# Kernel tuning notes

Hardware: AMD Instinct MI355X
Metric: run time of the kernel (lower is better)

Reference implementation:

```python
import jax, jax.numpy as jnp
import numpy as np

B, N, M, D, H, DK = 4, 2048, 1024, 512, 8, 64  # H*DK == D (required by residual E + E_)
SCALE = 1.0 / np.sqrt(DK)
NEG = -9e15


def setup_inputs() -> dict:
    key = jax.random.key(0)
    ks = jax.random.split(key, 24)
    def W(k, din, dout):
        return (0.02 * jax.random.truncated_normal(k, -2.0, 2.0, (din, dout))).astype(jnp.float32)
    inp = {
        'X': jax.random.normal(ks[0], (B, N, D), jnp.float32),
        'incidence_matrix': jax.random.randint(ks[1], (B, N, M), 0, 2, jnp.int32),
        'attn_bias': jnp.zeros((1,), jnp.float32),
        'E': jax.random.normal(ks[2], (B, M, D), jnp.float32),
        'Wqn': W(ks[3], D, H * DK), 'bqn': jnp.zeros((H * DK,), jnp.float32),
        'Wkn': W(ks[4], D, H * DK), 'bkn': jnp.zeros((H * DK,), jnp.float32),
        'Wvn': W(ks[5], D, H * DK), 'bvn': jnp.zeros((H * DK,), jnp.float32),
        'Wqe': W(ks[6], D, H * DK), 'bqe': jnp.zeros((H * DK,), jnp.float32),
        'Wke': W(ks[7], D, H * DK), 'bke': jnp.zeros((H * DK,), jnp.float32),
        'Wve': W(ks[8], D, H * DK), 'bve': jnp.zeros((H * DK,), jnp.float32),
        'Wm1': W(ks[9], D, D), 'bm1': jnp.zeros((D,), jnp.float32),
        'Wm2': W(ks[10], D, D), 'bm2': jnp.zeros((D,), jnp.float32),
        'g_ln': jnp.ones((D,), jnp.float32), 'b_ln': jnp.zeros((D,), jnp.float32),
    }
    return inp


def _heads(x, Wt, b):
    # [B, L, D] -> [B, H, L, DK]
    b_, l_ = x.shape[0], x.shape[1]
    return (x @ Wt + b).reshape(b_, l_, H, DK).transpose(0, 2, 1, 3)


def _merge(x):
    # [B, H, L, DK] -> [B, L, H*DK]
    b_, _, l_, _ = x.shape
    return x.transpose(0, 2, 1, 3).reshape(b_, l_, H * DK)


def _layernorm(x, g, b, eps=1e-7):
    mu = jnp.mean(x, axis=-1, keepdims=True)
    var = jnp.var(x, axis=-1, keepdims=True)
    return (x - mu) * jax.lax.rsqrt(var + eps) * g + b


def _gelu(x):
    return jax.nn.gelu(x, approximate=False)


def reference(X, incidence_matrix, attn_bias, E,
              Wqn, bqn, Wkn, bkn, Wvn, bvn,
              Wqe, bqe, Wke, bke, Wve, bve,
              Wm1, bm1, Wm2, bm2, g_ln, b_ln):
    q_n = _heads(X, Wqn, bqn)   # [B,H,N,DK]
    k_n = _heads(X, Wkn, bkn)
    v_n = _heads(X, Wvn, bvn)
    q_e = _heads(E, Wqe, bqe)   # [B,H,M,DK]

    # edge attends over nodes: [B,H,M,N], masked by incidence^T
    att_e = jnp.einsum('bhmd,bhnd->bhmn', q_e, k_n) * SCALE
    mask_e = (incidence_matrix > 0).transpose(0, 2, 1)[:, None, :, :]  # [B,1,M,N]
    att_e = jnp.where(mask_e, att_e, NEG)
    w_e = jax.nn.softmax(att_e, axis=-1)
    E_ = _gelu(jnp.einsum('bhmn,bhnd->bhmd', w_e, v_n))
    E_ = _merge(E_)                                   # [B,M,D]
    E_ = _layernorm(E + E_, g_ln, b_ln)
    E_ = _gelu(E_ @ Wm1 + bm1) @ Wm2 + bm2            # MLP

    k_e = _heads(E_, Wke, bke)  # [B,H,M,DK]
    v_e = _heads(E_, Wve, bve)

    # node attends over edges: [B,H,N,M], masked by incidence
    att_n = jnp.einsum('bhnd,bhmd->bhnm', q_n, k_e) * SCALE
    mask_n = (incidence_matrix > 0)[:, None, :, :]    # [B,1,N,M]
    att_n = jnp.where(mask_n, att_n, NEG)
    w_n = jax.nn.softmax(att_n, axis=-1)
    X_ = _gelu(jnp.einsum('bhnm,bhmd->bhnd', w_n, v_e))
    X_ = _merge(X_)                                   # [B,N,D]
    return (X_, E_)
```

## Files before the change

kernel.cpp:

```cpp
#include <hip/hip_runtime.h>

typedef unsigned short u16;
typedef unsigned int   u32;
typedef unsigned long long u64;

typedef __attribute__((ext_vector_type(8))) short  bf16x8;
typedef __attribute__((ext_vector_type(16))) float f32x16;

#define SC2 0.1803368801111243f
#define CS2 11.541560327111707f

__device__ __forceinline__ float bf2f(u16 h) { return __uint_as_float(((u32)h) << 16); }
__device__ __forceinline__ u16 f2bf(float f) {
  u32 u = __float_as_uint(f);
  return (u16)((u + 0x7FFFu + ((u >> 16) & 1u)) >> 16);
}
__device__ __forceinline__ float gelu_f(float x) {
  return 0.5f * x * (1.0f + erff(x * 0.70710678118654752440f));
}
__device__ __forceinline__ void dma16(const u16* g, u16* l) {
  __builtin_amdgcn_global_load_lds(
      (const __attribute__((address_space(1))) u32*)g,
      (__attribute__((address_space(3))) u32*)l, 16, 0, 0);
}
__device__ __forceinline__ u32 cvtpk(float lo, float hi) {
  u32 r;
  asm("v_cvt_pk_bf16_f32 %0, %1, %2" : "=v"(r) : "v"(lo), "v"(hi));
  return r;
}

__global__ void detect_dtype(const u16* __restrict__ X, u32* __restrict__ flag) {
  int lane = threadIdx.x;
  int bad = 0;
  #pragma unroll
  for (int i = 0; i < 8; ++i) {
    u16 v = X[i * 64 + lane];
    int e = (v >> 7) & 0xFF;
    if (e >= 0x88) bad++;
  }
  #pragma unroll
  for (int o = 1; o < 64; o <<= 1) bad += __shfl_xor(bad, o);
  if (lane == 0) *flag = (bad > 16) ? 1u : 0u;
}

__global__ __launch_bounds__(256) void fill_diag(u32* __restrict__ out, float base,
                                                 const u32* __restrict__ flag) {
  float v = base + (*flag ? 4000.0f : 0.0f);
  u16 h = f2bf(v);
  out[blockIdx.x * 256 + threadIdx.x] = (u32)h | ((u32)h << 16);
}

__global__ __launch_bounds__(256) void prep_all(
    const void* __restrict__ Xsrc, const void* __restrict__ Esrc,
    const int* __restrict__ inc,
    const void* w0, const void* w1, const void* w2, const void* w3,
    const void* w4, const void* w5, const void* w6, const void* w7,
    const void* p0, const void* p1, const void* p2, const void* p3, const void* p4,
    const void* p5, const void* p6, const void* p7, const void* p8, const void* p9,
    u16* __restrict__ XB, u16* __restrict__ EB, u16* __restrict__ WT,
    u16* __restrict__ VEC, u16* __restrict__ T0, u16* __restrict__ T1,
    const u32* __restrict__ flag) {
  int bi = blockIdx.x;
  int t = threadIdx.x;
  int fl = (int)(*flag);

  if (bi < 3072) {
    const void* src = bi < 2048 ? Xsrc : Esrc;
    u16* dst = bi < 2048 ? XB : EB;
    int base = bi < 2048 ? bi : bi - 2048;
    int i = (base * 256 + t) * 8;
    if (fl) {
      const float* s = (const float*)src + i;
      float4 a = *(const float4*)s;
      float4 b = *(const float4*)(s + 4);
      uint4 o;
      o.x = (u32)f2bf(a.x) | ((u32)f2bf(a.y) << 16);
      o.y = (u32)f2bf(a.z) | ((u32)f2bf(a.w) << 16);
      o.z = (u32)f2bf(b.x) | ((u32)f2bf(b.y) << 16);
      o.w = (u32)f2bf(b.z) | ((u32)f2bf(b.w) << 16);
      *(uint4*)(dst + i) = o;
    } else {
      *(uint4*)(dst + i) = *(const uint4*)((const u16*)src + i);
    }
  } else if (bi < 5120) {
    const void* wsrc[8] = {w0, w1, w2, w3, w4, w5, w6, w7};
    __shared__ u16 tile[32][33];
    int r = bi - 3072;
    int bx = (r & 15) * 32, by = ((r >> 4) & 15) * 32, z = r >> 8;
    const void* W = wsrc[z];
    u16* Wt = WT + (size_t)z * 262144;
    int tx = t & 31, ty = t >> 5;
    #pragma unroll
    for (int i = 0; i < 4; ++i) {
      int rr = ty + 8 * i;
      size_t src = (size_t)(by + rr) * 512 + bx + tx;
      tile[rr][tx] = fl ? f2bf(((const float*)W)[src]) : ((const u16*)W)[src];
    }
    __syncthreads();
    #pragma unroll
    for (int i = 0; i < 4; ++i) {
      int rr = ty + 8 * i;
      Wt[(size_t)(bx + rr) * 512 + by + tx] = tile[tx][rr];
    }
  } else if (bi == 5120) {
    const void* ps[10] = {p0, p1, p2, p3, p4, p5, p6, p7, p8, p9};
    for (int idx = t; idx < 5120; idx += 256) {
      int slot = idx >> 9, off = idx & 511;
      u16 v;
      if (fl) v = f2bf(((const float*)ps[slot])[off]);
      else    v = ((const u16*)ps[slot])[off];
      VEC[idx] = v;
    }
  } else {
    int r = bi - 5121;
    int qt32 = r & 31, nt = (r >> 5) & 31, b = r >> 10;
    int f = t >> 6, l = t & 63;
    int nl = l & 31, h = l >> 5;
    int key  = ((f >> 1) << 5) + nl;
    int qrow = ((f & 1) << 4) + h * 8;
    const int* src = inc + ((size_t)(b * 2048 + nt * 64 + key)) * 1024 + qt32 * 32 + qrow;
    uint4 a = *(const uint4*)src;
    uint4 c = *(const uint4*)(src + 4);
    uint4 o;
    o.x = (a.x ? 0u : 0xC480u) | (a.y ? 0u : 0xC4800000u);
    o.y = (a.z ? 0u : 0xC480u) | (a.w ? 0u : 0xC4800000u);
    o.z = (c.x ? 0u : 0xC480u) | (c.y ? 0u : 0xC4800000u);
    o.w = (c.z ? 0u : 0xC480u) | (c.w ? 0u : 0xC4800000u);
    u16* dst = (b < 2 ? T0 + (size_t)b * 2097152 : T1 + (size_t)(b - 2) * 2097152)
               + ((size_t)nt * 32 + qt32) * 2048 + t * 8;
    *(uint4*)dst = o;
  }
}

__global__ __launch_bounds__(256) void transposeV(const u16* __restrict__ Vp,
                                                  u16* __restrict__ VT, int Lk) {
  __shared__ u16 tile[64][72];
  int t = threadIdx.x;
  int nt = blockIdx.x;
  int bh = blockIdx.y;
  int nw = Lk >> 6;
  const u16* src = Vp + ((size_t)bh * Lk + nt * 64) * 64;
  int key = t >> 2, seg = t & 3;
  int dc0 = seg * 2, dc1 = seg * 2 + 1;
  uint4 a  = *(const uint4*)(src + key * 64 + ((dc0 ^ (key & 7)) << 3));
  uint4 b2 = *(const uint4*)(src + key * 64 + ((dc1 ^ (key & 7)) << 3));
  *(uint4*)&tile[key][dc0 * 8] = a;
  *(uint4*)&tile[key][dc1 * 8] = b2;
  __syncthreads();
  int d = t >> 2;
  u32 wb[8];
  #pragma unroll
  for (int i = 0; i < 8; ++i) {
    u32 lo = tile[seg * 16 + 2 * i][d];
    u32 hi = tile[seg * 16 + 2 * i + 1][d];
    wb[i] = lo | (hi << 16);
  }
  u16* base = VT + (((size_t)bh * nw + nt) * 64 + d) * 64;
  int kc0 = seg * 2, kc1 = seg * 2 + 1;
  uint4 o0; o0.x = wb[0]; o0.y = wb[1]; o0.z = wb[2]; o0.w = wb[3];
  uint4 o1; o1.x = wb[4]; o1.y = wb[5]; o1.z = wb[6]; o1.w = wb[7];
  *(uint4*)(base + ((kc0 ^ (d & 7)) << 3)) = o0;
  *(uint4*)(base + ((kc1 ^ (d & 7)) << 3)) = o1;
}

__global__ __launch_bounds__(256) void inc_tiles_node(const int* __restrict__ inc,
                                                      u16* __restrict__ T0,
                                                      u16* __restrict__ T1) {
  int qt32 = blockIdx.x, nt = blockIdx.y, b = blockIdx.z;
  int t = threadIdx.x;
  int f = t >> 6, l = t & 63;
  int nl = l & 31, h = l >> 5;
  int key  = ((f >> 1) << 5) + nl;
  int qrow = ((f & 1) << 4) + h * 8;
  const int* src = inc + ((size_t)(b * 2048 + qt32 * 32 + qrow)) * 1024 + nt * 64 + key;
  u16 o[8];
  #pragma unroll
  for (int e = 0; e < 8; ++e)
    o[e] = src[(size_t)e * 1024] ? (u16)0 : (u16)0xC480;
  uint4 ov;
  ov.x = (u32)o[0] | ((u32)o[1] << 16);
  ov.y = (u32)o[2] | ((u32)o[3] << 16);
  ov.z = (u32)o[4] | ((u32)o[5] << 16);
  ov.w = (u32)o[6] | ((u32)o[7] << 16);
  u16* dst = (b < 3 ? T0 + (size_t)b * 2097152 : T1)
             + ((size_t)nt * 64 + qt32) * 2048 + t * 8;
  *(uint4*)dst = ov;
}

__global__ __launch_bounds__(256) void gemm_tiled(const u16* __restrict__ A,
                                                  const u16* __restrict__ Wt0, u32 wtStride,
                                                  const u16* __restrict__ bias0, u32 bStride,
                                                  u16* __restrict__ C0, u32 cStride,
                                                  int act, int blocksPerMat,
                                                  u32 modeMask, int lkshift,
                                                  void* __restrict__ out2, size_t out2_off,
                                                  const u16* __restrict__ A3,
                                                  const u32* __restrict__ flag) {
  __shared__ u16 As[2][8192];
  __shared__ u16 Bs[2][8192];
  int wid = (blockIdx.x & 7) * (int)(gridDim.x >> 3) + (blockIdx.x >> 3);
  int mat = wid / blocksPerMat;
  int blk = wid % blocksPerMat;
  const u16* Wt = Wt0 + (size_t)mat * wtStride;
  const u16* bias = bias0 + (size_t)mat * bStride;
  u16* C = C0 + (size_t)mat * cStride;
  int mode = (modeMask >> mat) & 1u;
  int f32o = out2 ? (int)(*flag) : 0;
  const u16* Am = (A3 && mat == 3) ? A3 : A;
  int tm = blk >> 2, tn = blk & 3;
  int m0 = tm * 128, n0 = tn * 128;

  int t = threadIdx.x;
  int wave = t >> 6, lane = t & 63;
  int nl = lane & 31, h32 = lane >> 5;
  int wm = wave >> 1, wn = wave & 1;

  int srow = lane >> 3;
  int gch  = (lane & 7) ^ srow;
  const u16* Ab = Am + ((size_t)m0 + wave * 32) * 512 + (size_t)srow * 512 + gch * 8;
  const u16* Bb = Wt + ((size_t)n0 + wave * 32) * 512 + (size_t)srow * 512 + gch * 8;
  u16* AsW = &As[0][0] + wave * 32 * 64;
  u16* BsW = &Bs[0][0] + wave * 32 * 64;

  #pragma unroll
  for (int c = 0; c < 4; ++c) {
    dma16(Ab + (size_t)c * 8 * 512, AsW + c * 8 * 64);
    dma16(Bb + (size_t)c * 8 * 512, BsW + c * 8 * 64);
  }
  __syncthreads();

  f32x16 a00 = {}, a01 = {}, a10 = {}, a11 = {};

  for (int kk = 0; kk < 8; ++kk) {
    int buf = kk & 1;
    if (kk + 1 < 8) {
      int k0n = (kk + 1) * 64;
      u16* AD = &As[buf ^ 1][0] + wave * 32 * 64;
      u16* BD = &Bs[buf ^ 1][0] + wave * 32 * 64;
      #pragma unroll
      for (int c = 0; c < 4; ++c) {
        dma16(Ab + (size_t)c * 8 * 512 + k0n, AD + c * 8 * 64);
        dma16(Bb + (size_t)c * 8 * 512 + k0n, BD + c * 8 * 64);
      }
    }
    const u16* Ab_s = &As[buf][0];
    const u16* Bb_s = &Bs[buf][0];
    int ar0 = wm * 64 + nl, ar1 = wm * 64 + 32 + nl;
    int br0 = wn * 64 + nl, br1 = wn * 64 + 32 + nl;
    #pragma unroll
    for (int ks = 0; ks < 4; ++ks) {
      int sw = (((ks * 2 + h32) ^ (nl & 7)) << 3);
      bf16x8 fa0 = *(const bf16x8*)(Ab_s + ar0 * 64 + sw);
      bf16x8 fa1 = *(const bf16x8*)(Ab_s + ar1 * 64 + sw);
      bf16x8 fb0 = *(const bf16x8*)(Bb_s + br0 * 64 + sw);
      bf16x8 fb1 = *(const bf16x8*)(Bb_s + br1 * 64 + sw);
      a00 = __builtin_amdgcn_mfma_f32_32x32x16_bf16(fa0, fb0, a00, 0, 0, 0);
      a01 = __builtin_amdgcn_mfma_f32_32x32x16_bf16(fa0, fb1, a01, 0, 0, 0);
      a10 = __builtin_amdgcn_mfma_f32_32x32x16_bf16(fa1, fb0, a10, 0, 0, 0);
      a11 = __builtin_amdgcn_mfma_f32_32x32x16_bf16(fa1, fb1, a11, 0, 0, 0);
    }
    __syncthreads();
  }

  int nw = 1 << (lkshift - 6);
  #pragma unroll
  for (int am = 0; am < 2; ++am) {
    #pragma unroll
    for (int bn = 0; bn < 2; ++bn) {
      const f32x16* accp = am == 0 ? (bn == 0 ? &a00 : &a01)
                                   : (bn == 0 ? &a10 : &a11);
      f32x16 acc = *accp;
      int cn = n0 + wn * 64 + bn * 32 + nl;
      float bv = bf2f(bias[cn]);
      #pragma unroll
      for (int g = 0; g < 16; ++g) {
        int rm = m0 + wm * 64 + am * 32 + (g & 3) + 8 * (g >> 2) + 4 * h32;
        float v = acc[g] + bv;
        if (act) v = gelu_f(v);
        if (mode) {
          int bb = rm >> lkshift;
          int key = rm & ((1 << lkshift) - 1);
          int nt = key >> 6, kl = key & 63;
          int d = cn & 63;
          size_t ad = ((((size_t)bb * 8 + (cn >> 6)) * nw + nt) * 64 + kl) * 64
                      + (((d >> 3) ^ (kl & 7)) << 3) + (d & 7);
          C[ad] = f2bf(v);
        } else {
          size_t ad = (size_t)rm * 512 + cn;
          C[ad] = f2bf(v);
          if (out2) {
            if (f32o) ((float*)out2)[out2_off + ad] = v;
            else      ((u16*)out2)[out2_off + ad] = f2bf(v);
          }
        }
      }
    }
  }
}

__global__ __launch_bounds__(256, 4) void flash_mfma(
    const u16* __restrict__ Q,
    const u16* __restrict__ Kp,
    const u16* __restrict__ VTp,
    const u16* __restrict__ IncA,
    const u16* __restrict__ IncB,
    int nbA,
    void* __restrict__ Outv,
    u16* __restrict__ Opart, float* __restrict__ Lpart,
    int Lq, int Lk, int splits, int is_final, const u32* __restrict__ flag) {
  __shared__ u16 K_s[3][4096];
  __shared__ u16 V_s[3][4096];
  __shared__ u16 P_s[4][2048];

  int t = threadIdx.x;
  int wave = t >> 6, lane = t & 63;
  int nl = lane & 31, h32 = lane >> 5;
  int qtiles = Lq >> 7;
  int nwords = Lk >> 6;
  int chunk = (int)(gridDim.x >> 3);
  int wid = (blockIdx.x & 7) * chunk + (blockIdx.x >> 3);
  int r2 = wid % (qtiles * 32);
  int split = wid / (qtiles * 32);
  int qt = r2 % qtiles;
  int bh = r2 / qtiles;
  int h = bh & 7, b = bh >> 3;
  int row0 = qt * 128 + wave * 32;
  int per = nwords / splits;
  int tile0 = split * per;
  int f32o = is_final ? (int)(*flag) : 0;

  bf16x8 qf[4];
  {
    const u16* qp = Q + ((size_t)(b * Lq) + row0 + nl) * 512 + h * 64 + h32 * 8;
    #pragma unroll
    for (int ks = 0; ks < 4; ++ks) qf[ks] = *(const bf16x8*)(qp + ks * 16);
  }
  bf16x8 b0f = {}, b16f = {};
  #pragma unroll
  for (int e = 0; e < 8; ++e) {
    b0f[e]  = (nl == h32 * 8 + e)      ? (short)0x3F80 : (short)0;
    b16f[e] = (nl == 16 + h32 * 8 + e) ? (short)0x3F80 : (short)0;
  }

  const u16* Kbh = Kp + (size_t)bh * Lk * 64;
  const u16* Vbh = VTp + (size_t)bh * nwords * 4096;
  size_t tstr = (size_t)(Lq >> 5) * 2048;
  int qt2 = row0 >> 5;
  const u16* It = (b < nbA ? IncA + (size_t)b * 2097152
                           : IncB + (size_t)(b - nbA) * 2097152)
                  + (size_t)qt2 * 2048 + lane * 8;

  f32x16 o0 = {}, o1 = {};
  float lsum = 0.f;

  {
    const u16* TK = Kbh + (size_t)tile0 * 4096;
    const u16* TV = Vbh + (size_t)tile0 * 4096;
    #pragma unroll
    for (int c = 0; c < 2; ++c) {
      int ch = c * 4 + wave;
      dma16(TK + ch * 512 + lane * 8, &K_s[0][ch * 512]);
      dma16(TV + ch * 512 + lane * 8, &V_s[0][ch * 512]);
    }
    asm volatile("" ::: "memory");
    if (per > 1) {
      const u16* TK1 = TK + 4096;
      const u16* TV1 = TV + 4096;
      #pragma unroll
      for (int c = 0; c < 2; ++c) {
        int ch = c * 4 + wave;
        dma16(TK1 + ch * 512 + lane * 8, &K_s[1][ch * 512]);
        dma16(TV1 + ch * 512 + lane * 8, &V_s[1][ch * 512]);
      }
    }
    asm volatile("" ::: "memory");
  }
  bf16x8 mc0, mc1, mc2, mc3;
  {
    const u16* p = It + (size_t)tile0 * tstr;
    mc0 = *(const bf16x8*)(p);
    mc1 = *(const bf16x8*)(p + 512);
    mc2 = *(const bf16x8*)(p + 1024);
    mc3 = *(const bf16x8*)(p + 1536);
  }
  __syncthreads();

  for (int i = 0; i < per; ++i) {
    int nt = tile0 + i;
    int bi = i % 3;
    bf16x8 mn0, mn1, mn2, mn3;
    if (i + 2 < per) {
      int bd = (i + 2) % 3;
      const u16* TK = Kbh + (size_t)(nt + 2) * 4096;
      const u16* TV = Vbh + (size_t)(nt + 2) * 4096;
      #pragma unroll
      for (int c = 0; c < 2; ++c) {
        int ch = c * 4 + wave;
        dma16(TK + ch * 512 + lane * 8, &K_s[bd][ch * 512]);
        dma16(TV + ch * 512 + lane * 8, &V_s[bd][ch * 512]);
      }
    }
    asm volatile("" ::: "memory");
    if (i + 1 < per) {
      const u16* p = It + (size_t)(nt + 1) * tstr;
      mn0 = *(const bf16x8*)(p);
      mn1 = *(const bf16x8*)(p + 512);
      mn2 = *(const bf16x8*)(p + 1024);
      mn3 = *(const bf16x8*)(p + 1536);
    }

    f32x16 s0 = {}, s1 = {};
    #pragma unroll
    for (int ks = 0; ks < 4; ++ks) {
      int ch = ks * 2 + h32;
      bf16x8 k0 = *(const bf16x8*)&K_s[bi][nl * 64 + ((ch ^ (nl & 7)) << 3)];
      bf16x8 k1 = *(const bf16x8*)&K_s[bi][(32 + nl) * 64 + ((ch ^ (nl & 7)) << 3)];
      s0 = __builtin_amdgcn_mfma_f32_32x32x16_bf16(k0, qf[ks], s0, 0, 0, 0);
      s1 = __builtin_amdgcn_mfma_f32_32x32x16_bf16(k1, qf[ks], s1, 0, 0, 0);
    }
    s0 = __builtin_amdgcn_mfma_f32_32x32x16_bf16(mc0, b0f,  s0, 0, 0, 0);
    s0 = __builtin_amdgcn_mfma_f32_32x32x16_bf16(mc1, b16f, s0, 0, 0, 0);
    s1 = __builtin_amdgcn_mfma_f32_32x32x16_bf16(mc2, b0f,  s1, 0, 0, 0);
    s1 = __builtin_amdgcn_mfma_f32_32x32x16_bf16(mc3, b16f, s1, 0, 0, 0);

    #pragma unroll
    for (int gg = 0; gg < 4; ++gg) {
      float pv0[4], pv1[4];
      #pragma unroll
      for (int r = 0; r < 4; ++r) {
        int g = gg * 4 + r;
        float e0 = exp2f(fmaf(s0[g], SC2, -CS2));
        float e1 = exp2f(fmaf(s1[g], SC2, -CS2));
        pv0[r] = e0;
        pv1[r] = e1;
        lsum += e0 + e1;
      }
      uint2 a0, a1;
      a0.x = cvtpk(pv0[0], pv0[1]);
      a0.y = cvtpk(pv0[2], pv0[3]);
      a1.x = cvtpk(pv1[0], pv1[1]);
      a1.y = cvtpk(pv1[2], pv1[3]);
      *(uint2*)&P_s[wave][gg * 256 + nl * 8 + 4 * h32]       = a0;
      *(uint2*)&P_s[wave][(4 + gg) * 256 + nl * 8 + 4 * h32] = a1;
    }
    asm volatile("s_waitcnt lgkmcnt(0)" ::: "memory");
    #pragma unroll
    for (int ks2 = 0; ks2 < 4; ++ks2) {
      int ch = ks2 * 2 + h32;
      bf16x8 pf = *(const bf16x8*)&P_s[wave][ch * 256 + nl * 8];
      bf16x8 v0 = *(const bf16x8*)&V_s[bi][nl * 64 + ((ch ^ (nl & 7)) << 3)];
      bf16x8 v1 = *(const bf16x8*)&V_s[bi][(32 + nl) * 64 + ((ch ^ (nl & 7)) << 3)];
      o0 = __builtin_amdgcn_mfma_f32_32x32x16_bf16(pf, v0, o0, 0, 0, 0);
      o1 = __builtin_amdgcn_mfma_f32_32x32x16_bf16(pf, v1, o1, 0, 0, 0);
    }
    mc0 = mn0; mc1 = mn1; mc2 = mn2; mc3 = mn3;
    asm volatile("s_waitcnt vmcnt(8)" ::: "memory");
    __builtin_amdgcn_s_barrier();
  }
  lsum += __shfl_xor(lsum, 32);

  if (Opart) {
    u16* ob = Opart + (size_t)split * 2097152;
    #pragma unroll
    for (int g = 0; g < 16; ++g) {
      int m = (g & 3) + 8 * (g >> 2) + 4 * h32;
      size_t base = ((size_t)(b * Lq) + row0 + m) * 512 + h * 64;
      ob[base + nl]      = f2bf(o0[g]);
      ob[base + 32 + nl] = f2bf(o1[g]);
    }
    if (h32 == 0)
      Lpart[(size_t)split * 32768 + ((size_t)(b * Lq) + row0 + nl) * 8 + h] = lsum;
  } else {
    #pragma unroll
    for (int g = 0; g < 16; ++g) {
      int m = (g & 3) + 8 * (g >> 2) + 4 * h32;
      float lv = __shfl(lsum, m);
      float inv = 1.0f / (lv + 1e-30f);
      size_t base = ((size_t)(b * Lq) + row0 + m) * 512 + h * 64;
      float v0 = gelu_f(o0[g] * inv);
      float v1 = gelu_f(o1[g] * inv);
      if (f32o) {
        ((float*)Outv)[base + nl]      = v0;
        ((float*)Outv)[base + 32 + nl] = v1;
      } else {
        ((u16*)Outv)[base + nl]      = f2bf(v0);
        ((u16*)Outv)[base + 32 + nl] = f2bf(v1);
      }
    }
  }
}

__global__ __launch_bounds__(256) void ln_fused(const u16* __restrict__ Op,
                                                const float* __restrict__ Lp,
                                                const u16* __restrict__ E,
                                                const u16* __restrict__ g,
                                                const u16* __restrict__ bb,
                                                u16* __restrict__ out) {
  int r = blockIdx.x;
  int t = threadIdx.x;
  int e = t * 2;
  int h = e >> 6;
  float lv = Lp[r * 8 + h] + Lp[32768 + r * 8 + h] + 1e-30f;
  float inv = 1.0f / lv;
  size_t idx = (size_t)r * 512 + e;
  u32 u0 = *(const u32*)&Op[idx];
  u32 u1 = *(const u32*)&Op[2097152 + idx];
  u32 ue = *(const u32*)&E[idx];
  float x0 = bf2f((u16)(ue & 0xffffu)) +
             gelu_f((bf2f((u16)(u0 & 0xffffu)) + bf2f((u16)(u1 & 0xffffu))) * inv);
  float x1 = bf2f((u16)(ue >> 16)) +
             gelu_f((bf2f((u16)(u0 >> 16)) + bf2f((u16)(u1 >> 16))) * inv);
  float s = x0 + x1, q = x0 * x0 + x1 * x1;
  #pragma unroll
  for (int o = 32; o; o >>= 1) { s += __shfl_down(s, o); q += __shfl_down(q, o); }
  __shared__ float red[8];
  int wv = t >> 6, ln = t & 63;
  if (ln == 0) { red[wv] = s; red[4 + wv] = q; }
  __syncthreads();
  s = red[0] + red[1] + red[2] + red[3];
  q = red[4] + red[5] + red[6] + red[7];
  float mean = s * (1.f / 512.f);
  float var  = q * (1.f / 512.f) - mean * mean;
  float rs = rsqrtf(var + 1e-7f);
  u32 ug = *(const u32*)(g + e);
  u32 ub = *(const u32*)(bb + e);
  float y0 = (x0 - mean) * rs * bf2f((u16)(ug & 0xffffu)) + bf2f((u16)(ub & 0xffffu));
  float y1 = (x1 - mean) * rs * bf2f((u16)(ug >> 16)) + bf2f((u16)(ub >> 16));
  *(u32*)(out + idx) = (u32)f2bf(y0) | ((u32)f2bf(y1) << 16);
}

extern "C" void kernel_launch(void* const* d_in, const int* in_sizes, int n_in,
                              void* d_out, int out_size, void* d_ws, size_t ws_size,
                              hipStream_t stream) {
  (void)in_sizes; (void)n_in; (void)out_size;
  const int* inc = (const int*)d_in[1];

  char* ws = (char*)d_ws;
  u32* FLAG = (u32*)ws;
  u16* VEC  = (u16*)(ws + 1024);
  u16* WT   = (u16*)(ws + 65536);
  u16* XB   = (u16*)(ws + 8454144);
  u16* EB   = (u16*)(ws + 16842752);
  u16* QN   = (u16*)(ws + 21037056);
  u16* KN   = (u16*)(ws + 29425664);
  u16* VN   = (u16*)(ws + 37814272);
  u16* QE   = (u16*)(ws + 46202880);
  u16* EATT = (u16*)(ws + 50397184);
  u16* EFIN = (u16*)(ws + 54591488);
  const size_t NEEDED = 60882944;
  u16* ELN = (u16*)(ws + 29425664);
  u16* H1  = (u16*)(ws + 33619968);
  u16* KE  = (u16*)(ws + 37814272);
  u16* Opart = XB;
  float* Lpart = (float*)(ws + 4259840);
  u16* ETIL0 = EATT;
  u16* ETIL1 = (u16*)d_out + 4194304;
  u16* NTIL0 = XB;
  u16* NTIL1 = QE;
  u16* VTn = (u16*)d_out;
  u16* VTe = EATT;
  u16* VE  = (u16*)(ws + 42008576);

  detect_dtype<<<1, 64, 0, stream>>>((const u16*)d_in[0], FLAG);

  if (ws_size < NEEDED) {
    fill_diag<<<8192, 256, 0, stream>>>((u32*)d_out,
                                        1000.0f + (float)(ws_size >> 20), FLAG);
    return;
  }

  prep_all<<<9217, 256, 0, stream>>>(
      d_in[0], d_in[3], inc,
      d_in[4], d_in[6], d_in[8], d_in[10], d_in[12], d_in[14], d_in[16], d_in[18],
      d_in[5], d_in[7], d_in[9], d_in[11], d_in[13], d_in[15], d_in[17], d_in[19],
      d_in[20], d_in[21],
      XB, EB, WT, VEC, ETIL0, ETIL1, FLAG);

  gemm_tiled<<<896, 256, 0, stream>>>(XB, WT, 262144, VEC, 512,
                                      QN, 4194304, 0, 256, 0b0110u, 11,
                                      nullptr, 0, EB, FLAG);

  transposeV<<<dim3(32, 32), 256, 0, stream>>>(VN, VTn, 2048);

  flash_mfma<<<512, 256, 0, stream>>>(QE, KN, VTn, ETIL0, ETIL1, 2, nullptr,
                                      Opart, Lpart, 1024, 2048, 2, 0, FLAG);

  ln_fused<<<4096, 256, 0, stream>>>(Opart, Lpart, EB,
                                     VEC + 8 * 512, VEC + 9 * 512, ELN);

  inc_tiles_node<<<dim3(64, 16, 4), 256, 0, stream>>>(inc, NTIL0, NTIL1);

  gemm_tiled<<<128, 256, 0, stream>>>(ELN, WT + 6 * 262144, 0, VEC + 6 * 512, 0,
                                      H1, 0, 1, 128, 0, 11, nullptr, 0,
                                      nullptr, FLAG);
  gemm_tiled<<<128, 256, 0, stream>>>(H1, WT + 7 * 262144, 0, VEC + 7 * 512, 0,
                                      EFIN, 0, 0, 128, 0, 11,
                                      d_out, 4194304, nullptr, FLAG);

  gemm_tiled<<<256, 256, 0, stream>>>(EFIN, WT + 4 * 262144, 262144, VEC + 4 * 512, 512,
                                      KE, 2097152, 0, 128, 0b11u, 10,
                                      nullptr, 0, nullptr, FLAG);
  transposeV<<<dim3(16, 32), 256, 0, stream>>>(VE, VTe, 1024);

  flash_mfma<<<512, 256, 0, stream>>>(QN, KE, VTe, NTIL0, NTIL1, 3, d_out,
                                      nullptr, nullptr, 2048, 1024, 1, 1, FLAG);
}
```

Baseline: 349.8 us.

## Fuse V transpose into projection GEMM epilogue and restructure flash K/V pipeline

```diff
diff --git a/kernel.cpp b/kernel.cpp
--- a/kernel.cpp
+++ b/kernel.cpp
@@ -132,37 +132,6 @@
   }
 }
 
-__global__ __launch_bounds__(256) void transposeV(const u16* __restrict__ Vp,
-                                                  u16* __restrict__ VT, int Lk) {
-  __shared__ u16 tile[64][72];
-  int t = threadIdx.x;
-  int nt = blockIdx.x;
-  int bh = blockIdx.y;
-  int nw = Lk >> 6;
-  const u16* src = Vp + ((size_t)bh * Lk + nt * 64) * 64;
-  int key = t >> 2, seg = t & 3;
-  int dc0 = seg * 2, dc1 = seg * 2 + 1;
-  uint4 a  = *(const uint4*)(src + key * 64 + ((dc0 ^ (key & 7)) << 3));
-  uint4 b2 = *(const uint4*)(src + key * 64 + ((dc1 ^ (key & 7)) << 3));
-  *(uint4*)&tile[key][dc0 * 8] = a;
-  *(uint4*)&tile[key][dc1 * 8] = b2;
-  __syncthreads();
-  int d = t >> 2;
-  u32 wb[8];
-  #pragma unroll
-  for (int i = 0; i < 8; ++i) {
-    u32 lo = tile[seg * 16 + 2 * i][d];
-    u32 hi = tile[seg * 16 + 2 * i + 1][d];
-    wb[i] = lo | (hi << 16);
-  }
-  u16* base = VT + (((size_t)bh * nw + nt) * 64 + d) * 64;
-  int kc0 = seg * 2, kc1 = seg * 2 + 1;
-  uint4 o0; o0.x = wb[0]; o0.y = wb[1]; o0.z = wb[2]; o0.w = wb[3];
-  uint4 o1; o1.x = wb[4]; o1.y = wb[5]; o1.z = wb[6]; o1.w = wb[7];
-  *(uint4*)(base + ((kc0 ^ (d & 7)) << 3)) = o0;
-  *(uint4*)(base + ((kc1 ^ (d & 7)) << 3)) = o1;
-}
-
 __global__ __launch_bounds__(256) void inc_tiles_node(const int* __restrict__ inc,
                                                       u16* __restrict__ T0,
                                                       u16* __restrict__ T1) {
@@ -195,6 +164,7 @@
                                                   u32 modeMask, int lkshift,
                                                   void* __restrict__ out2, size_t out2_off,
                                                   const u16* __restrict__ A3,
+                                                  u16* __restrict__ Cvt,
                                                   const u32* __restrict__ flag) {
   __shared__ u16 As[2][8192];
   __shared__ u16 Bs[2][8192];
@@ -204,7 +174,7 @@
   const u16* Wt = Wt0 + (size_t)mat * wtStride;
   const u16* bias = bias0 + (size_t)mat * bStride;
   u16* C = C0 + (size_t)mat * cStride;
-  int mode = (modeMask >> mat) & 1u;
+  int mode = (int)((modeMask >> (mat * 2)) & 3u);
   int f32o = out2 ? (int)(*flag) : 0;
   const u16* Am = (A3 && mat == 3) ? A3 : A;
   int tm = blk >> 2, tn = blk & 3;
@@ -277,7 +247,7 @@
         int rm = m0 + wm * 64 + am * 32 + (g & 3) + 8 * (g >> 2) + 4 * h32;
         float v = acc[g] + bv;
         if (act) v = gelu_f(v);
-        if (mode) {
+        if (mode == 1) {
           int bb = rm >> lkshift;
           int key = rm & ((1 << lkshift) - 1);
           int nt = key >> 6, kl = key & 63;
@@ -285,6 +255,14 @@
           size_t ad = ((((size_t)bb * 8 + (cn >> 6)) * nw + nt) * 64 + kl) * 64
                       + (((d >> 3) ^ (kl & 7)) << 3) + (d & 7);
           C[ad] = f2bf(v);
+        } else if (mode == 2) {
+          int bb = rm >> lkshift;
+          int key = rm & ((1 << lkshift) - 1);
+          int nt = key >> 6, kl = key & 63;
+          int d = cn & 63;
+          size_t ad = ((((size_t)bb * 8 + (cn >> 6)) * nw + nt) * 64 + d) * 64
+                      + (((kl >> 3) ^ (d & 7)) << 3) + (kl & 7);
+          Cvt[ad] = f2bf(v);
         } else {
           size_t ad = (size_t)rm * 512 + cn;
           C[ad] = f2bf(v);
@@ -298,7 +276,7 @@
   }
 }
 
-__global__ __launch_bounds__(256, 4) void flash_mfma(
+__global__ __launch_bounds__(256, 2) void flash_mfma(
     const u16* __restrict__ Q,
     const u16* __restrict__ Kp,
     const u16* __restrict__ VTp,
@@ -308,8 +286,8 @@
     void* __restrict__ Outv,
     u16* __restrict__ Opart, float* __restrict__ Lpart,
     int Lq, int Lk, int splits, int is_final, const u32* __restrict__ flag) {
-  __shared__ u16 K_s[3][4096];
-  __shared__ u16 V_s[3][4096];
+  __shared__ u16 K_s[2][8192];
+  __shared__ u16 V_s[2][8192];
   __shared__ u16 P_s[4][2048];
 
   int t = threadIdx.x;
@@ -317,8 +295,8 @@
   int nl = lane & 31, h32 = lane >> 5;
   int qtiles = Lq >> 7;
   int nwords = Lk >> 6;
-  int chunk = (int)(gridDim.x >> 3);
-  int wid = (blockIdx.x & 7) * chunk + (blockIdx.x >> 3);
+  int chunkg = (int)(gridDim.x >> 3);
+  int wid = (blockIdx.x & 7) * chunkg + (blockIdx.x >> 3);
   int r2 = wid % (qtiles * 32);
   int split = wid / (qtiles * 32);
   int qt = r2 % qtiles;
@@ -345,10 +323,9 @@
   const u16* Kbh = Kp + (size_t)bh * Lk * 64;
   const u16* Vbh = VTp + (size_t)bh * nwords * 4096;
   size_t tstr = (size_t)(Lq >> 5) * 2048;
-  int qt2 = row0 >> 5;
   const u16* It = (b < nbA ? IncA + (size_t)b * 2097152
                            : IncB + (size_t)(b - nbA) * 2097152)
-                  + (size_t)qt2 * 2048 + lane * 8;
+                  + (size_t)(row0 >> 5) * 2048 + lane * 8;
 
   f32x16 o0 = {}, o1 = {};
   float lsum = 0.f;
@@ -357,105 +334,103 @@
     const u16* TK = Kbh + (size_t)tile0 * 4096;
     const u16* TV = Vbh + (size_t)tile0 * 4096;
     #pragma unroll
-    for (int c = 0; c < 2; ++c) {
+    for (int c = 0; c < 4; ++c) {
       int ch = c * 4 + wave;
       dma16(TK + ch * 512 + lane * 8, &K_s[0][ch * 512]);
       dma16(TV + ch * 512 + lane * 8, &V_s[0][ch * 512]);
     }
-    asm volatile("" ::: "memory");
-    if (per > 1) {
-      const u16* TK1 = TK + 4096;
-      const u16* TV1 = TV + 4096;
+  }
+  bf16x8 mc0, mc1, mc2, mc3, mc4, mc5, mc6, mc7;
+  {
+    const u16* p0 = It + (size_t)tile0 * tstr;
+    const u16* p1 = p0 + tstr;
+    mc0 = *(const bf16x8*)(p0);        mc1 = *(const bf16x8*)(p0 + 512);
+    mc2 = *(const bf16x8*)(p0 + 1024); mc3 = *(const bf16x8*)(p0 + 1536);
+    mc4 = *(const bf16x8*)(p1);        mc5 = *(const bf16x8*)(p1 + 512);
+    mc6 = *(const bf16x8*)(p1 + 1024); mc7 = *(const bf16x8*)(p1 + 1536);
+  }
+  __syncthreads();
+
+  int nch = per >> 1;
+  for (int cc = 0; cc < nch; ++cc) {
+    int buf = cc & 1;
+    int nt0 = tile0 + cc * 2;
+    bf16x8 mn0, mn1, mn2, mn3, mn4, mn5, mn6, mn7;
+    if (cc + 1 < nch) {
+      const u16* TK = Kbh + (size_t)(nt0 + 2) * 4096;
+      const u16* TV = Vbh + (size_t)(nt0 + 2) * 4096;
       #pragma unroll
-      for (int c = 0; c < 2; ++c) {
+      for (int c = 0; c < 4; ++c) {
         int ch = c * 4 + wave;
-        dma16(TK1 + ch * 512 + lane * 8, &K_s[1][ch * 512]);
-        dma16(TV1 + ch * 512 + lane * 8, &V_s[1][ch * 512]);
-      }
-    }
-    asm volatile("" ::: "memory");
-  }
-  bf16x8 mc0, mc1, mc2, mc3;
-  {
-    const u16* p = It + (size_t)tile0 * tstr;
-    mc0 = *(const bf16x8*)(p);
-    mc1 = *(const bf16x8*)(p + 512);
-    mc2 = *(const bf16x8*)(p + 1024);
-    mc3 = *(const bf16x8*)(p + 1536);
-  }
-  __syncthreads();
-
-  for (int i = 0; i < per; ++i) {
-    int nt = tile0 + i;
-    int bi = i % 3;
-    bf16x8 mn0, mn1, mn2, mn3;
-    if (i + 2 < per) {
-      int bd = (i + 2) % 3;
-      const u16* TK = Kbh + (size_t)(nt + 2) * 4096;
-      const u16* TV = Vbh + (size_t)(nt + 2) * 4096;
+        dma16(TK + ch * 512 + lane * 8, &K_s[buf ^ 1][ch * 512]);
+        dma16(TV + ch * 512 + lane * 8, &V_s[buf ^ 1][ch * 512]);
+      }
+      asm volatile("" ::: "memory");
+      const u16* p0 = It + (size_t)(nt0 + 2) * tstr;
+      const u16* p1 = p0 + tstr;
+      mn0 = *(const bf16x8*)(p0);        mn1 = *(const bf16x8*)(p0 + 512);
+      mn2 = *(const bf16x8*)(p0 + 1024); mn3 = *(const bf16x8*)(p0 + 1536);
+      mn4 = *(const bf16x8*)(p1);        mn5 = *(const bf16x8*)(p1 + 512);
+      mn6 = *(const bf16x8*)(p1 + 1024); mn7 = *(const bf16x8*)(p1 + 1536);
+    }
+
+    #pragma unroll
+    for (int j = 0; j < 2; ++j) {
+      const u16* Kb = &K_s[buf][j * 4096];
+      const u16* Vb = &V_s[buf][j * 4096];
+      bf16x8 m0j = j ? mc4 : mc0;
+      bf16x8 m1j = j ? mc5 : mc1;
+      bf16x8 m2j = j ? mc6 : mc2;
+      bf16x8 m3j = j ? mc7 : mc3;
+
+      f32x16 s0 = {}, s1 = {};
       #pragma unroll
-      for (int c = 0; c < 2; ++c) {
-        int ch = c * 4 + wave;
-        dma16(TK + ch * 512 + lane * 8, &K_s[bd][ch * 512]);
-        dma16(TV + ch * 512 + lane * 8, &V_s[bd][ch * 512]);
-      }
-    }
-    asm volatile("" ::: "memory");
-    if (i + 1 < per) {
-      const u16* p = It + (size_t)(nt + 1) * tstr;
-      mn0 = *(const bf16x8*)(p);
-      mn1 = *(const bf16x8*)(p + 512);
-      mn2 = *(const bf16x8*)(p + 1024);
-      mn3 = *(const bf16x8*)(p + 1536);
-    }
-
-    f32x16 s0 = {}, s1 = {};
-    #pragma unroll
-    for (int ks = 0; ks < 4; ++ks) {
-      int ch = ks * 2 + h32;
-      bf16x8 k0 = *(const bf16x8*)&K_s[bi][nl * 64 + ((ch ^ (nl & 7)) << 3)];
-      bf16x8 k1 = *(const bf16x8*)&K_s[bi][(32 + nl) * 64 + ((ch ^ (nl & 7)) << 3)];
-      s0 = __builtin_amdgcn_mfma_f32_32x32x16_bf16(k0, qf[ks], s0, 0, 0, 0);
-      s1 = __builtin_amdgcn_mfma_f32_32x32x16_bf16(k1, qf[ks], s1, 0, 0, 0);
-    }
-    s0 = __builtin_amdgcn_mfma_f32_32x32x16_bf16(mc0, b0f,  s0, 0, 0, 0);
-    s0 = __builtin_amdgcn_mfma_f32_32x32x16_bf16(mc1, b16f, s0, 0, 0, 0);
-    s1 = __builtin_amdgcn_mfma_f32_32x32x16_bf16(mc2, b0f,  s1, 0, 0, 0);
-    s1 = __builtin_amdgcn_mfma_f32_32x32x16_bf16(mc3, b16f, s1, 0, 0, 0);
-
-    #pragma unroll
-    for (int gg = 0; gg < 4; ++gg) {
-      float pv0[4], pv1[4];
+      for (int ks = 0; ks < 4; ++ks) {
+        int ch = ks * 2 + h32;
+        bf16x8 k0 = *(const bf16x8*)&Kb[nl * 64 + ((ch ^ (nl & 7)) << 3)];
+        bf16x8 k1 = *(const bf16x8*)&Kb[(32 + nl) * 64 + ((ch ^ (nl & 7)) << 3)];
+        s0 = __builtin_amdgcn_mfma_f32_32x32x16_bf16(k0, qf[ks], s0, 0, 0, 0);
+        s1 = __builtin_amdgcn_mfma_f32_32x32x16_bf16(k1, qf[ks], s1, 0, 0, 0);
+      }
+      s0 = __builtin_amdgcn_mfma_f32_32x32x16_bf16(m0j, b0f,  s0, 0, 0, 0);
+      s0 = __builtin_amdgcn_mfma_f32_32x32x16_bf16(m1j, b16f, s0, 0, 0, 0);
+      s1 = __builtin_amdgcn_mfma_f32_32x32x16_bf16(m2j, b0f,  s1, 0, 0, 0);
+      s1 = __builtin_amdgcn_mfma_f32_32x32x16_bf16(m3j, b16f, s1, 0, 0, 0);
+
       #pragma unroll
-      for (int r = 0; r < 4; ++r) {
-        int g = gg * 4 + r;
-        float e0 = exp2f(fmaf(s0[g], SC2, -CS2));
-        float e1 = exp2f(fmaf(s1[g], SC2, -CS2));
-        pv0[r] = e0;
-        pv1[r] = e1;
-        lsum += e0 + e1;
-      }
-      uint2 a0, a1;
-      a0.x = cvtpk(pv0[0], pv0[1]);
-      a0.y = cvtpk(pv0[2], pv0[3]);
-      a1.x = cvtpk(pv1[0], pv1[1]);
-      a1.y = cvtpk(pv1[2], pv1[3]);
-      *(uint2*)&P_s[wave][gg * 256 + nl * 8 + 4 * h32]       = a0;
-      *(uint2*)&P_s[wave][(4 + gg) * 256 + nl * 8 + 4 * h32] = a1;
-    }
-    asm volatile("s_waitcnt lgkmcnt(0)" ::: "memory");
-    #pragma unroll
-    for (int ks2 = 0; ks2 < 4; ++ks2) {
-      int ch = ks2 * 2 + h32;
-      bf16x8 pf = *(const bf16x8*)&P_s[wave][ch * 256 + nl * 8];
-      bf16x8 v0 = *(const bf16x8*)&V_s[bi][nl * 64 + ((ch ^ (nl & 7)) << 3)];
-      bf16x8 v1 = *(const bf16x8*)&V_s[bi][(32 + nl) * 64 + ((ch ^ (nl & 7)) << 3)];
-      o0 = __builtin_amdgcn_mfma_f32_32x32x16_bf16(pf, v0, o0, 0, 0, 0);
-      o1 = __builtin_amdgcn_mfma_f32_32x32x16_bf16(pf, v1, o1, 0, 0, 0);
+      for (int gg = 0; gg < 4; ++gg) {
+        float pv0[4], pv1[4];
+        #pragma unroll
+        for (int r = 0; r < 4; ++r) {
+          int g = gg * 4 + r;
+          float e0 = exp2f(fmaf(s0[g], SC2, -CS2));
+          float e1 = exp2f(fmaf(s1[g], SC2, -CS2));
+          pv0[r] = e0;
+          pv1[r] = e1;
+          lsum += e0 + e1;
+        }
+        uint2 a0, a1;
+        a0.x = cvtpk(pv0[0], pv0[1]);
+        a0.y = cvtpk(pv0[2], pv0[3]);
+        a1.x = cvtpk(pv1[0], pv1[1]);
+        a1.y = cvtpk(pv1[2], pv1[3]);
+        *(uint2*)&P_s[wave][gg * 256 + nl * 8 + 4 * h32]       = a0;
+        *(uint2*)&P_s[wave][(4 + gg) * 256 + nl * 8 + 4 * h32] = a1;
+      }
+      asm volatile("s_waitcnt lgkmcnt(0)" ::: "memory");
+      #pragma unroll
+      for (int ks2 = 0; ks2 < 4; ++ks2) {
+        int ch = ks2 * 2 + h32;
+        bf16x8 pf = *(const bf16x8*)&P_s[wave][ch * 256 + nl * 8];
+        bf16x8 v0 = *(const bf16x8*)&Vb[nl * 64 + ((ch ^ (nl & 7)) << 3)];
+        bf16x8 v1 = *(const bf16x8*)&Vb[(32 + nl) * 64 + ((ch ^ (nl & 7)) << 3)];
+        o0 = __builtin_amdgcn_mfma_f32_32x32x16_bf16(pf, v0, o0, 0, 0, 0);
+        o1 = __builtin_amdgcn_mfma_f32_32x32x16_bf16(pf, v1, o1, 0, 0, 0);
+      }
     }
     mc0 = mn0; mc1 = mn1; mc2 = mn2; mc3 = mn3;
-    asm volatile("s_waitcnt vmcnt(8)" ::: "memory");
-    __builtin_amdgcn_s_barrier();
+    mc4 = mn4; mc5 = mn5; mc6 = mn6; mc7 = mn7;
+    __syncthreads();
   }
   lsum += __shfl_xor(lsum, 32);
 
@@ -543,7 +518,6 @@
   u16* EB   = (u16*)(ws + 16842752);
   u16* QN   = (u16*)(ws + 21037056);
   u16* KN   = (u16*)(ws + 29425664);
-  u16* VN   = (u16*)(ws + 37814272);
   u16* QE   = (u16*)(ws + 46202880);
   u16* EATT = (u16*)(ws + 50397184);
   u16* EFIN = (u16*)(ws + 54591488);
@@ -559,7 +533,6 @@
   u16* NTIL1 = QE;
   u16* VTn = (u16*)d_out;
   u16* VTe = EATT;
-  u16* VE  = (u16*)(ws + 42008576);
 
   detect_dtype<<<1, 64, 0, stream>>>((const u16*)d_in[0], FLAG);
 
@@ -577,10 +550,8 @@
       XB, EB, WT, VEC, ETIL0, ETIL1, FLAG);
 
   gemm_tiled<<<896, 256, 0, stream>>>(XB, WT, 262144, VEC, 512,
-                                      QN, 4194304, 0, 256, 0b0110u, 11,
-                                      nullptr, 0, EB, FLAG);
-
-  transposeV<<<dim3(32, 32), 256, 0, stream>>>(VN, VTn, 2048);
+                                      QN, 4194304, 0, 256, 0x24u, 11,
+                                      nullptr, 0, EB, VTn, FLAG);
 
   flash_mfma<<<512, 256, 0, stream>>>(QE, KN, VTn, ETIL0, ETIL1, 2, nullptr,
                                       Opart, Lpart, 1024, 2048, 2, 0, FLAG);
@@ -592,15 +563,14 @@
 
   gemm_tiled<<<128, 256, 0, stream>>>(ELN, WT + 6 * 262144, 0, VEC + 6 * 512, 0,
                                       H1, 0, 1, 128, 0, 11, nullptr, 0,
-                                      nullptr, FLAG);
+                                      nullptr, nullptr, FLAG);
   gemm_tiled<<<128, 256, 0, stream>>>(H1, WT + 7 * 262144, 0, VEC + 7 * 512, 0,
                                       EFIN, 0, 0, 128, 0, 11,
-                                      d_out, 4194304, nullptr, FLAG);
+                                      d_out, 4194304, nullptr, nullptr, FLAG);
 
   gemm_tiled<<<256, 256, 0, stream>>>(EFIN, WT + 4 * 262144, 262144, VEC + 4 * 512, 512,
-                                      KE, 2097152, 0, 128, 0b11u, 10,
-                                      nullptr, 0, nullptr, FLAG);
-  transposeV<<<dim3(16, 32), 256, 0, stream>>>(VE, VTe, 1024);
+                                      KE, 2097152, 0, 128, 0x9u, 10,
+                                      nullptr, 0, nullptr, VTe, FLAG);
 
   flash_mfma<<<512, 256, 0, stream>>>(QN, KE, VTe, NTIL0, NTIL1, 3, d_out,
                                       nullptr, nullptr, 2048, 1024, 1, 1, FLAG);
```

After: 458.3 us. 31.0% more time.
